# Kernel tuning notes

Hardware: AMD Instinct MI355X
Metric: run time of the kernel (lower is better)

Reference implementation:

```python
import jax, jax.numpy as jnp
import numpy as np

DIM = 768
HEADS = 12
HIDDEN = 4 * DIM
EPS = 1e-5


def _layer_norm(x, g, b):
    mu = jnp.mean(x, axis=-1, keepdims=True)
    var = jnp.mean(jnp.square(x - mu), axis=-1, keepdims=True)
    return (x - mu) * jax.lax.rsqrt(var + EPS) * g + b


def setup_inputs() -> dict:
    key = jax.random.key(0)
    ks = jax.random.split(key, 10)
    B, N, C = 16, 1024, DIM
    s = lambda fan: 1.0 / np.sqrt(fan)
    return {
        "x": jax.random.normal(ks[0], (B, N, C), dtype=jnp.float32),
        "ln1_g": jnp.ones((C,), jnp.float32),
        "ln1_b": jnp.zeros((C,), jnp.float32),
        "qkv_w": jax.random.normal(ks[1], (C, 3 * C), jnp.float32) * s(C),
        "qkv_b": jnp.zeros((3 * C,), jnp.float32),
        "proj_w": jax.random.normal(ks[2], (C, C), jnp.float32) * s(C),
        "proj_b": jnp.zeros((C,), jnp.float32),
        "ln2_g": jnp.ones((C,), jnp.float32),
        "ln2_b": jnp.zeros((C,), jnp.float32),
        "fc1_w": jax.random.normal(ks[3], (C, HIDDEN), jnp.float32) * s(C),
        "fc1_b": jnp.zeros((HIDDEN,), jnp.float32),
        "fc2_w": jax.random.normal(ks[4], (HIDDEN, C), jnp.float32) * s(HIDDEN),
        "fc2_b": jnp.zeros((C,), jnp.float32),
    }


def reference(x, ln1_g, ln1_b, qkv_w, qkv_b, proj_w, proj_b,
              ln2_g, ln2_b, fc1_w, fc1_b, fc2_w, fc2_b):
    B, N, C = x.shape
    Hd = C // HEADS
    scale = Hd ** -0.5

    # --- attention branch (pre-norm) ---
    h = _layer_norm(x, ln1_g, ln1_b)
    qkv = h @ qkv_w + qkv_b                       # [B,N,3C]
    qkv = qkv.reshape(B, N, 3, HEADS, Hd).transpose(2, 0, 3, 1, 4)
    q, k, v = qkv[0], qkv[1], qkv[2]              # [B,H,N,Hd]
    attn = jnp.einsum("bhqd,bhkd->bhqk", q, k) * scale
    attn = jax.nn.softmax(attn, axis=-1)
    o = jnp.einsum("bhqk,bhkd->bhqd", attn, v)    # [B,H,N,Hd]
    o = o.transpose(0, 2, 1, 3).reshape(B, N, C)
    x = x + (o @ proj_w + proj_b)

    # --- MLP branch (pre-norm) ---
    h = _layer_norm(x, ln2_g, ln2_b)
    h = jax.nn.gelu(h @ fc1_w + fc1_b, approximate=False)
    x = x + (h @ fc2_w + fc2_b)
    return x
```

## Files before the change

### kernel.cpp

```cpp
#include <hip/hip_runtime.h>

typedef __bf16 bf16x8 __attribute__((ext_vector_type(8)));
typedef __bf16 bf16x4 __attribute__((ext_vector_type(4)));
typedef float f32x4 __attribute__((ext_vector_type(4)));
typedef float f32x16 __attribute__((ext_vector_type(16)));

#define MFMA16(a,b,c) __builtin_amdgcn_mfma_f32_16x16x32_bf16((a),(b),(c),0,0,0)
#define MFMA32(a,b,c) __builtin_amdgcn_mfma_f32_32x32x16_bf16((a),(b),(c),0,0,0)
#define EXP2R(x) __builtin_amdgcn_exp2f(x)

#define BB   16
#define SEQ  1024
#define CD   768
#define NHD  12
#define HDD  64
#define HID  3072
#define MT   (BB*SEQ)

__device__ __forceinline__ void gload16(const void* g, void* l) {
    __builtin_amdgcn_global_load_lds(
        (const __attribute__((address_space(1))) void*)g,
        (__attribute__((address_space(3))) void*)l, 16, 0, 0);
}

__device__ __forceinline__ unsigned pk2(float lo, float hi) {
    unsigned short a = __builtin_bit_cast(unsigned short, (__bf16)lo);
    unsigned short b = __builtin_bit_cast(unsigned short, (__bf16)hi);
    return (unsigned)a | ((unsigned)b << 16);
}

__device__ __forceinline__ float fast_gelu(float x) {
    float u = x * x * x;
    float y = fmaf(0.044715f, u, x);
    float e = EXP2R(-2.3022083f * y);
    return x * __builtin_amdgcn_rcpf(1.0f + e);
}

__global__ __launch_bounds__(256)
void transpose_w(const float* __restrict__ W, __bf16* __restrict__ WT, int R, int C)
{
    __shared__ float t[32][33];
    int tc = C >> 5;
    int bid = blockIdx.x;
    int br = bid / tc, bc = bid % tc;
    int x = threadIdx.x & 31, y = threadIdx.x >> 5;
#pragma unroll
    for (int i = 0; i < 4; ++i)
        t[y + 8*i][x] = W[(size_t)(br*32 + y + 8*i)*C + bc*32 + x];
    __syncthreads();
#pragma unroll
    for (int i = 0; i < 4; ++i)
        WT[(size_t)(bc*32 + y + 8*i)*R + br*32 + x] = (__bf16)t[x][y + 8*i];
}

__global__ __launch_bounds__(256)
void ln_kernel(const float* __restrict__ xin, const float* __restrict__ g,
               const float* __restrict__ bb, __bf16* out)
{
    int row = blockIdx.x * 4 + (threadIdx.x >> 6);
    int lane = threadIdx.x & 63;
    const float* xr = xin + (size_t)row * CD + lane * 4;
    float4 v0 = *(const float4*)(xr);
    float4 v1 = *(const float4*)(xr + 256);
    float4 v2 = *(const float4*)(xr + 512);
    float s = v0.x+v0.y+v0.z+v0.w + v1.x+v1.y+v1.z+v1.w + v2.x+v2.y+v2.z+v2.w;
#pragma unroll
    for (int off = 1; off < 64; off <<= 1) s += __shfl_xor(s, off);
    float mu = s * (1.0f/768.0f);
    float q =
        (v0.x-mu)*(v0.x-mu)+(v0.y-mu)*(v0.y-mu)+(v0.z-mu)*(v0.z-mu)+(v0.w-mu)*(v0.w-mu)+
        (v1.x-mu)*(v1.x-mu)+(v1.y-mu)*(v1.y-mu)+(v1.z-mu)*(v1.z-mu)+(v1.w-mu)*(v1.w-mu)+
        (v2.x-mu)*(v2.x-mu)+(v2.y-mu)*(v2.y-mu)+(v2.z-mu)*(v2.z-mu)+(v2.w-mu)*(v2.w-mu);
#pragma unroll
    for (int off = 1; off < 64; off <<= 1) q += __shfl_xor(q, off);
    float rstd = rsqrtf(q * (1.0f/768.0f) + 1e-5f);

    __bf16* orow = out + (size_t)row * CD + lane * 4;
#pragma unroll
    for (int p = 0; p < 3; ++p) {
        float4 xv = (p == 0) ? v0 : (p == 1) ? v1 : v2;
        float4 gv = *(const float4*)(g  + p*256 + lane*4);
        float4 bv = *(const float4*)(bb + p*256 + lane*4);
        bf16x4 ov;
        ov[0] = (__bf16)((xv.x-mu)*rstd*gv.x + bv.x);
        ov[1] = (__bf16)((xv.y-mu)*rstd*gv.y + bv.y);
        ov[2] = (__bf16)((xv.z-mu)*rstd*gv.z + bv.z);
        ov[3] = (__bf16)((xv.w-mu)*rstd*gv.w + bv.w);
        *(bf16x4*)(orow + p*256) = ov;
    }
}

template<int EPI>
__global__ __launch_bounds__(512)
void gemm_bt(const __bf16* __restrict__ A, const __bf16* __restrict__ BT,
             const float* __restrict__ bias,
             const float* res, float* outf,
             __bf16* __restrict__ outb,
             __bf16* __restrict__ qb, __bf16* __restrict__ kb, __bf16* __restrict__ vb,
             int M, int N, int K)
{
    __shared__ alignas(16) __bf16 lsA[2][128*64];
    __shared__ alignas(16) __bf16 lsB[2][128*64];

    int nbn = N >> 7;
    int nwg = (M >> 7) * nbn;
    int bid = (int)blockIdx.x;
    int cpx = nwg >> 3;
    int sw = (bid & 7) * cpx + (bid >> 3);
    int bm = sw / nbn, bn = sw % nbn;
    int row0 = bm << 7, col0 = bn << 7;

    int tid = threadIdx.x;
    int lane = tid & 63, w = tid >> 6;
    int wr = w >> 2, wc = w & 3;
    int lr = lane & 15, lg = lane >> 4;

    f32x4 acc[4][2] = {};
    int swz = (lr & 7) << 4;

    auto stage = [&](int buf, int ktE) {
#pragma unroll
        for (int i = 0; i < 2; ++i) {
            int s = tid*16 + (i << 13);
            int r = s >> 7;
            int ch = ((s >> 4) & 7) ^ (r & 7);
            gload16(A  + (size_t)(row0 + r)*K + (ktE + ch*8),
                    (char*)lsA + buf*16384 + w*1024 + (i << 13));
            gload16(BT + (size_t)(col0 + r)*K + (ktE + ch*8),
                    (char*)lsB + buf*16384 + w*1024 + (i << 13));
        }
    };

    int nkt = K >> 6;
    stage(0, 0);
    __syncthreads();
    int cur = 0;

    for (int kt = 0; kt < nkt; ++kt) {
        if (kt + 1 < nkt) stage(cur ^ 1, (kt + 1) << 6);

        const char* lA = (const char*)lsA + cur*16384;
        const char* lB = (const char*)lsB + cur*16384;
#pragma unroll
        for (int ks = 0; ks < 2; ++ks) {
            int cb = (ks*64 + lg*16) ^ swz;
            bf16x8 af[4], bfv[2];
#pragma unroll
            for (int m = 0; m < 4; ++m)
                af[m] = *(const bf16x8*)(lA + (wr*64 + m*16 + lr)*128 + cb);
#pragma unroll
            for (int n = 0; n < 2; ++n)
                bfv[n] = *(const bf16x8*)(lB + (wc*32 + n*16 + lr)*128 + cb);
#pragma unroll
            for (int m = 0; m < 4; ++m)
#pragma unroll
                for (int n = 0; n < 2; ++n)
                    acc[m][n] = MFMA16(af[m], bfv[n], acc[m][n]);
        }
        __syncthreads();
        cur ^= 1;
    }

    int rbase = row0 + wr*64 + lg*4;
    int cbase = col0 + wc*32 + lr;
#pragma unroll
    for (int n = 0; n < 2; ++n) {
        int col = cbase + n*16;
        float bv = bias[col];
        if constexpr (EPI == 0) {
            int which = col / CD;
            int c2 = col - which * CD;
            int head = c2 >> 6, d = c2 & 63;
#pragma unroll
            for (int m = 0; m < 4; ++m) {
                int r0 = rbase + m*16;
                int b = r0 >> 10, nn = r0 & 1023;
                if (which == 2) {
                    bf16x4 pv;
#pragma unroll
                    for (int j = 0; j < 4; ++j) pv[j] = (__bf16)(acc[m][n][j] + bv);
                    *(bf16x4*)&vb[(((size_t)b*NHD + head)*HDD + d)*SEQ + nn] = pv;
                } else {
                    __bf16* dst = (which == 0) ? qb : kb;
#pragma unroll
                    for (int j = 0; j < 4; ++j)
                        dst[(((size_t)b*NHD + head)*SEQ + nn + j)*HDD + d] =
                            (__bf16)(acc[m][n][j] + bv);
                }
            }
        } else {
#pragma unroll
            for (int m = 0; m < 4; ++m) {
                int rr = rbase + m*16;
#pragma unroll
                for (int j = 0; j < 4; ++j) {
                    float val = acc[m][n][j] + bv;
                    int r = rr + j;
                    if constexpr (EPI == 1) {
                        outf[(size_t)r*N + col] = res[(size_t)r*N + col] + val;
                    } else {
                        outb[(size_t)r*N + col] = (__bf16)fast_gelu(val);
                    }
                }
            }
        }
    }
}

__global__ __launch_bounds__(256)
void attn_kernel(const __bf16* __restrict__ q, const __bf16* __restrict__ k,
                 const __bf16* __restrict__ vT, __bf16* __restrict__ o)
{
    __shared__ alignas(16) __bf16 kls[2][64*64];
    __shared__ alignas(16) __bf16 vls[2][64*64];

    int bid = blockIdx.x;
    int u = bid >> 3, x = bid & 7;
    int bh = x*24 + (u >> 3);
    int qt = u & 7;
    int b = bh / NHD, hh = bh % NHD;
    int tid = threadIdx.x, lane = tid & 63, w = tid >> 6;
    int lq = lane & 31, h = lane >> 5;

    int qg = qt*128 + w*32 + lq;
    const __bf16* qp = q + ((size_t)bh*SEQ + qg)*HDD + h*8;
    bf16x8 qf[4];
#pragma unroll
    for (int s = 0; s < 4; ++s) qf[s] = *(const bf16x8*)(qp + s*16);

    const __bf16* kbase = k  + (size_t)bh*SEQ*HDD;
    const __bf16* vbase = vT + (size_t)bh*HDD*SEQ;

    int srow0 = tid >> 3;
    int scol0 = ((tid & 7) ^ (srow0 & 7)) * 8;
    int srow1 = srow0 + 32;

    auto stage = [&](int buf, int kv) {
        char* kl = (char*)kls + buf*8192 + w*1024;
        char* vl = (char*)vls + buf*8192 + w*1024;
        gload16(kbase + (size_t)(kv + srow0)*HDD + scol0, kl);
        gload16(kbase + (size_t)(kv + srow1)*HDD + scol0, kl + 4096);
        gload16(vbase + (size_t)srow0*SEQ + kv + scol0, vl);
        gload16(vbase + (size_t)srow1*SEQ + kv + scol0, vl + 4096);
    };

    const float SCL2 = 0.125f * 1.44269504f;
    const float NB   = -12.0f * SCL2;
    float lrun = 0.f;
    f32x16 oa0 = {}, oa1 = {};

    stage(0, 0);
    __syncthreads();
    int cur = 0;
    int rswz = (lq & 7) << 4;

    for (int kt = 0; kt < SEQ/64; ++kt) {
        if (kt + 1 < SEQ/64) stage(cur ^ 1, (kt + 1)*64);

        const char* kc = (const char*)kls + cur*8192;
        const char* vc = (const char*)vls + cur*8192;

        bf16x8 ka0[4], ka1[4];
#pragma unroll
        for (int s = 0; s < 4; ++s) {
            int bc = (h*16 + s*32) ^ rswz;
            ka0[s] = *(const bf16x8*)(kc + lq*128 + bc);
            ka1[s] = *(const bf16x8*)(kc + (lq + 32)*128 + bc);
        }
        bf16x8 vf0[4], vf1[4];
#pragma unroll
        for (int g = 0; g < 4; ++g) {
            int bc = (h*16 + g*32) ^ rswz;
            vf0[g] = *(const bf16x8*)(vc + lq*128 + bc);
            vf1[g] = *(const bf16x8*)(vc + (lq + 32)*128 + bc);
        }

        f32x16 s0 = {}, s1 = {};
        __builtin_amdgcn_s_setprio(1);
#pragma unroll
        for (int s = 0; s < 4; ++s) {
            s0 = MFMA32(ka0[s], qf[s], s0);
            s1 = MFMA32(ka1[s], qf[s], s1);
        }
        __builtin_amdgcn_s_setprio(0);

#pragma unroll
        for (int i = 0; i < 16; ++i) s0[i] = EXP2R(fmaf(s0[i], SCL2, NB));
#pragma unroll
        for (int i = 0; i < 16; ++i) s1[i] = EXP2R(fmaf(s1[i], SCL2, NB));
        float a8[8];
#pragma unroll
        for (int i = 0; i < 8; ++i)
            a8[i] = (s0[i] + s0[i + 8]) + (s1[i] + s1[i + 8]);
        float s4a = (a8[0] + a8[1]) + (a8[2] + a8[3]);
        float s4b = (a8[4] + a8[5]) + (a8[6] + a8[7]);
        lrun += s4a + s4b;

#pragma unroll
        for (int t = 0; t < 2; ++t) {
            const f32x16& sp = t ? s1 : s0;
            unsigned d0 = pk2(sp[ 0], sp[ 1]);
            unsigned d1 = pk2(sp[ 2], sp[ 3]);
            unsigned d2 = pk2(sp[ 4], sp[ 5]);
            unsigned d3 = pk2(sp[ 6], sp[ 7]);
            unsigned d4 = pk2(sp[ 8], sp[ 9]);
            unsigned d5 = pk2(sp[10], sp[11]);
            unsigned d6 = pk2(sp[12], sp[13]);
            unsigned d7 = pk2(sp[14], sp[15]);
            unsigned pd0 = __shfl_xor(d0, 32), pd1 = __shfl_xor(d1, 32);
            unsigned pd2 = __shfl_xor(d2, 32), pd3 = __shfl_xor(d3, 32);
            unsigned pd4 = __shfl_xor(d4, 32), pd5 = __shfl_xor(d5, 32);
            unsigned pd6 = __shfl_xor(d6, 32), pd7 = __shfl_xor(d7, 32);
            union { unsigned u[4]; bf16x8 v; } f0, f1;
            f0.u[0] = h ? pd2 : d0;
            f0.u[1] = h ? pd3 : d1;
            f0.u[2] = h ? d2 : pd0;
            f0.u[3] = h ? d3 : pd1;
            f1.u[0] = h ? pd6 : d4;
            f1.u[1] = h ? pd7 : d5;
            f1.u[2] = h ? d6 : pd4;
            f1.u[3] = h ? d7 : pd5;
            __builtin_amdgcn_s_setprio(1);
            oa0 = MFMA32(vf0[t*2 + 0], f0.v, oa0);
            oa1 = MFMA32(vf1[t*2 + 0], f0.v, oa1);
            oa0 = MFMA32(vf0[t*2 + 1], f1.v, oa0);
            oa1 = MFMA32(vf1[t*2 + 1], f1.v, oa1);
            __builtin_amdgcn_s_setprio(0);
        }

        __syncthreads();
        cur ^= 1;
    }

    lrun += __shfl_xor(lrun, 32);
    float inv = __builtin_amdgcn_rcpf(lrun);
    oa0 = oa0 * inv;
    oa1 = oa1 * inv;
    __bf16* orow = o + ((size_t)b*SEQ + qg)*CD + hh*HDD;
#pragma unroll
    for (int dt = 0; dt < 2; ++dt) {
        f32x16 oa = dt ? oa1 : oa0;
        unsigned d0 = pk2(oa[ 0], oa[ 1]);
        unsigned d1 = pk2(oa[ 2], oa[ 3]);
        unsigned d2 = pk2(oa[ 4], oa[ 5]);
        unsigned d3 = pk2(oa[ 6], oa[ 7]);
        unsigned d4 = pk2(oa[ 8], oa[ 9]);
        unsigned d5 = pk2(oa[10], oa[11]);
        unsigned d6 = pk2(oa[12], oa[13]);
        unsigned d7 = pk2(oa[14], oa[15]);
        unsigned pd0 = __shfl_xor(d0, 32), pd1 = __shfl_xor(d1, 32);
        unsigned pd2 = __shfl_xor(d2, 32), pd3 = __shfl_xor(d3, 32);
        unsigned pd4 = __shfl_xor(d4, 32), pd5 = __shfl_xor(d5, 32);
        unsigned pd6 = __shfl_xor(d6, 32), pd7 = __shfl_xor(d7, 32);
        union { unsigned u[4]; bf16x8 v; } g0, g1;
        g0.u[0] = h ? pd2 : d0;
        g0.u[1] = h ? pd3 : d1;
        g0.u[2] = h ? d2 : pd0;
        g0.u[3] = h ? d3 : pd1;
        g1.u[0] = h ? pd6 : d4;
        g1.u[1] = h ? pd7 : d5;
        g1.u[2] = h ? d6 : pd4;
        g1.u[3] = h ? d7 : pd5;
        *(bf16x8*)(orow + dt*32 +  0 + h*8) = g0.v;
        *(bf16x8*)(orow + dt*32 + 16 + h*8) = g1.v;
    }
}

extern "C" void kernel_launch(void* const* d_in, const int* in_sizes, int n_in,
                              void* d_out, int out_size, void* d_ws, size_t ws_size,
                              hipStream_t stream)
{
    const float* x     = (const float*)d_in[0];
    const float* ln1g  = (const float*)d_in[1];
    const float* ln1b  = (const float*)d_in[2];
    const float* qkvw  = (const float*)d_in[3];
    const float* qkvb  = (const float*)d_in[4];
    const float* projw = (const float*)d_in[5];
    const float* projb = (const float*)d_in[6];
    const float* ln2g  = (const float*)d_in[7];
    const float* ln2b  = (const float*)d_in[8];
    const float* fc1w  = (const float*)d_in[9];
    const float* fc1b  = (const float*)d_in[10];
    const float* fc2w  = (const float*)d_in[11];
    const float* fc2b  = (const float*)d_in[12];
    float* out = (float*)d_out;

    char* p = (char*)d_ws;
    auto alloc = [&](size_t bytes) { char* r = p; p += (bytes + 255) & ~(size_t)255; return r; };
    __bf16* wqkvT  = (__bf16*)alloc((size_t)3*CD*CD*2);
    __bf16* wprojT = (__bf16*)alloc((size_t)CD*CD*2);
    __bf16* wfc1T  = (__bf16*)alloc((size_t)HID*CD*2);
    __bf16* wfc2T  = (__bf16*)alloc((size_t)CD*HID*2);
    __bf16* hbuf   = (__bf16*)alloc((size_t)MT*CD*2);
    __bf16* qbuf   = (__bf16*)alloc((size_t)BB*NHD*SEQ*HDD*2);
    __bf16* kbuf   = (__bf16*)alloc((size_t)BB*NHD*SEQ*HDD*2);
    __bf16* vtbuf  = (__bf16*)alloc((size_t)BB*NHD*SEQ*HDD*2);
    (void)alloc((size_t)BB*NHD*SEQ*HDD*2);
    __bf16* hhbuf  = qbuf;

    transpose_w<<<(CD/32)*(3*CD/32), 256, 0, stream>>>(qkvw,  wqkvT, CD, 3*CD);
    transpose_w<<<(CD/32)*(CD/32),   256, 0, stream>>>(projw, wprojT, CD, CD);
    transpose_w<<<(CD/32)*(HID/32),  256, 0, stream>>>(fc1w,  wfc1T, CD, HID);
    transpose_w<<<(HID/32)*(CD/32),  256, 0, stream>>>(fc2w,  wfc2T, HID, CD);

    ln_kernel<<<MT/4, 256, 0, stream>>>(x, ln1g, ln1b, hbuf);

    gemm_bt<0><<<(MT/128)*(3*CD/128), 512, 0, stream>>>(
        hbuf, wqkvT, qkvb, nullptr, nullptr, nullptr, qbuf, kbuf, vtbuf, MT, 3*CD, CD);

    attn_kernel<<<BB*NHD*8, 256, 0, stream>>>(qbuf, kbuf, vtbuf, hbuf);

    gemm_bt<1><<<(MT/128)*(CD/128), 512, 0, stream>>>(
        hbuf, wprojT, projb, x, out, nullptr, nullptr, nullptr, nullptr, MT, CD, CD);

    ln_kernel<<<MT/4, 256, 0, stream>>>(out, ln2g, ln2b, hbuf);

    gemm_bt<2><<<(MT/128)*(HID/128), 512, 0, stream>>>(
        hbuf, wfc1T, fc1b, nullptr, nullptr, hhbuf, nullptr, nullptr, nullptr, MT, HID, CD);

    gemm_bt<1><<<(MT/128)*(CD/128), 512, 0, stream>>>(
        hhbuf, wfc2T, fc2b, out, out, nullptr, nullptr, nullptr, nullptr, MT, CD, HID);
}
```

Baseline: 463.7 us.

## Add 256x256-tile GEMM for MLP layers and fuse weight transposes with LN1

Adds a new GEMM kernel with 256x256 output tiles per 512-thread workgroup. It double-buffers LDS with staged prefetch interleaved into the MFMA loop, and uses it for the fc1 and fc2 GEMMs to raise data reuse per tile. Separately, the four weight-transpose launches and the first layer norm are merged into one prep kernel to cut launch overhead. The larger tiles use 128 KB of LDS and more accumulator registers, and the fc2 GEMM gets only 192 workgroups, which may underfill the GPU.

```diff
diff --git a/kernel.cpp b/kernel.cpp
--- a/kernel.cpp
+++ b/kernel.cpp
@@ -8,6 +8,7 @@
 #define MFMA16(a,b,c) __builtin_amdgcn_mfma_f32_16x16x32_bf16((a),(b),(c),0,0,0)
 #define MFMA32(a,b,c) __builtin_amdgcn_mfma_f32_32x32x16_bf16((a),(b),(c),0,0,0)
 #define EXP2R(x) __builtin_amdgcn_exp2f(x)
+#define SBAR() asm volatile("s_barrier" ::: "memory")
 
 #define BB   16
 #define SEQ  1024
@@ -36,12 +37,11 @@
     return x * __builtin_amdgcn_rcpf(1.0f + e);
 }
 
-__global__ __launch_bounds__(256)
-void transpose_w(const float* __restrict__ W, __bf16* __restrict__ WT, int R, int C)
-{
-    __shared__ float t[32][33];
+__device__ __forceinline__ void transpose_body(
+    const float* __restrict__ W, __bf16* __restrict__ WT, int R, int C, int bid,
+    float (*t)[33])
+{
     int tc = C >> 5;
-    int bid = blockIdx.x;
     int br = bid / tc, bc = bid % tc;
     int x = threadIdx.x & 31, y = threadIdx.x >> 5;
 #pragma unroll
@@ -53,11 +53,11 @@
         WT[(size_t)(bc*32 + y + 8*i)*R + br*32 + x] = (__bf16)t[x][y + 8*i];
 }
 
-__global__ __launch_bounds__(256)
-void ln_kernel(const float* __restrict__ xin, const float* __restrict__ g,
-               const float* __restrict__ bb, __bf16* out)
-{
-    int row = blockIdx.x * 4 + (threadIdx.x >> 6);
+__device__ __forceinline__ void ln_body(
+    const float* __restrict__ xin, const float* __restrict__ g,
+    const float* __restrict__ bb, __bf16* out, int bid)
+{
+    int row = bid * 4 + ((int)threadIdx.x >> 6);
     int lane = threadIdx.x & 63;
     const float* xr = xin + (size_t)row * CD + lane * 4;
     float4 v0 = *(const float4*)(xr);
@@ -90,6 +90,31 @@
     }
 }
 
+__global__ __launch_bounds__(256)
+void prep_kernel(const float* qkvw, const float* projw, const float* fc1w, const float* fc2w,
+                 __bf16* wqkvT, __bf16* wprojT, __bf16* wfc1T, __bf16* wfc2T,
+                 const float* x, const float* g1, const float* b1, __bf16* hbuf)
+{
+    __shared__ float t[32][33];
+    int bid = blockIdx.x;
+    if (bid < 1728) { transpose_body(qkvw,  wqkvT,  CD,  3*CD, bid, t); return; }
+    bid -= 1728;
+    if (bid < 576)  { transpose_body(projw, wprojT, CD,  CD,   bid, t); return; }
+    bid -= 576;
+    if (bid < 2304) { transpose_body(fc1w,  wfc1T,  CD,  HID,  bid, t); return; }
+    bid -= 2304;
+    if (bid < 2304) { transpose_body(fc2w,  wfc2T,  HID, CD,   bid, t); return; }
+    bid -= 2304;
+    ln_body(x, g1, b1, hbuf, bid);
+}
+
+__global__ __launch_bounds__(256)
+void ln_kernel(const float* __restrict__ xin, const float* __restrict__ g,
+               const float* __restrict__ bb, __bf16* out)
+{
+    ln_body(xin, g, bb, out, blockIdx.x);
+}
+
 template<int EPI>
 __global__ __launch_bounds__(512)
 void gemm_bt(const __bf16* __restrict__ A, const __bf16* __restrict__ BT,
@@ -201,6 +226,118 @@
                     } else {
                         outb[(size_t)r*N + col] = (__bf16)fast_gelu(val);
                     }
+                }
+            }
+        }
+    }
+}
+
+template<int EPI>
+__global__ __launch_bounds__(512, 2)
+void gemm256(const __bf16* __restrict__ A, const __bf16* __restrict__ BT,
+             const float* __restrict__ bias,
+             const float* res, float* outf, __bf16* __restrict__ outb,
+             int M, int N, int K)
+{
+    __shared__ alignas(16) __bf16 lsA[2][256*64];
+    __shared__ alignas(16) __bf16 lsB[2][256*64];
+
+    int nbn = N >> 8;
+    int nwg = (M >> 8) * nbn;
+    int bid = (int)blockIdx.x;
+    int cpx = nwg >> 3;
+    int sw = (bid & 7) * cpx + (bid >> 3);
+    int bm = sw / nbn, bn = sw % nbn;
+    int row0 = bm << 8, col0 = bn << 8;
+
+    int tid = threadIdx.x;
+    int lane = tid & 63, w = tid >> 6;
+    int wr = w >> 2, wc = w & 3;
+    int lr = lane & 15, lg = lane >> 4;
+    int swz = (lr & 7) << 4;
+
+    const __bf16* Ab = A  + (size_t)row0 * K;
+    const __bf16* Bb = BT + (size_t)col0 * K;
+
+    auto stageH = [&](__bf16* ls, const __bf16* src, int half, int ktE) {
+#pragma unroll
+        for (int rd = 0; rd < 2; ++rd) {
+            int s = tid*16 + (rd << 13);
+            int r = s >> 7;
+            int ch = ((s >> 4) & 7) ^ (r & 7);
+            gload16(src + (size_t)(half*128 + r)*K + (ktE + ch*8),
+                    (char*)ls + half*16384 + (rd << 13) + w*1024);
+        }
+    };
+
+    f32x4 acc[8][4] = {};
+
+    int nkt = K >> 6;
+    stageH(lsA[0], Ab, 0, 0); stageH(lsA[0], Ab, 1, 0);
+    stageH(lsB[0], Bb, 0, 0); stageH(lsB[0], Bb, 1, 0);
+
+    for (int t = 0; t < nkt; ++t) {
+        int slot = t & 1, nslot = slot ^ 1;
+        int kn = (t + 1) << 6;
+        bool pf = (t + 1 < nkt);
+
+        if (pf) {
+            stageH(lsA[nslot], Ab, 0, kn);
+            asm volatile("s_waitcnt vmcnt(2)" ::: "memory");
+        } else {
+            asm volatile("s_waitcnt vmcnt(0)" ::: "memory");
+        }
+        SBAR();
+
+        const char* lA = (const char*)lsA[slot];
+        const char* lB = (const char*)lsB[slot];
+
+#pragma unroll
+        for (int ks = 0; ks < 2; ++ks) {
+            int cb = (ks*64 + lg*16) ^ swz;
+            bf16x8 bfr[4];
+#pragma unroll
+            for (int n = 0; n < 4; ++n)
+                bfr[n] = *(const bf16x8*)(lB + (wc*64 + n*16 + lr)*128 + cb);
+#pragma unroll
+            for (int mh = 0; mh < 2; ++mh) {
+                bf16x8 afr[4];
+#pragma unroll
+                for (int mm = 0; mm < 4; ++mm)
+                    afr[mm] = *(const bf16x8*)(lA + (wr*128 + mh*64 + mm*16 + lr)*128 + cb);
+                if (pf) {
+                    if (ks == 0 && mh == 0) stageH(lsA[nslot], Ab, 1, kn);
+                    else if (ks == 0 && mh == 1) stageH(lsB[nslot], Bb, 0, kn);
+                    else if (ks == 1 && mh == 0) stageH(lsB[nslot], Bb, 1, kn);
+                }
+                __builtin_amdgcn_s_setprio(1);
+#pragma unroll
+                for (int mm = 0; mm < 4; ++mm)
+#pragma unroll
+                    for (int n = 0; n < 4; ++n)
+                        acc[mh*4 + mm][n] = MFMA16(afr[mm], bfr[n], acc[mh*4 + mm][n]);
+                __builtin_amdgcn_s_setprio(0);
+            }
+        }
+        SBAR();
+    }
+
+    int rb = row0 + wr*128 + lg*4;
+    int cb2 = col0 + wc*64 + lr;
+#pragma unroll
+    for (int n = 0; n < 4; ++n) {
+        int col = cb2 + n*16;
+        float bv = bias[col];
+#pragma unroll
+        for (int m = 0; m < 8; ++m) {
+#pragma unroll
+            for (int j = 0; j < 4; ++j) {
+                int r = rb + m*16 + j;
+                float val = acc[m][n][j] + bv;
+                if constexpr (EPI == 1) {
+                    outf[(size_t)r*N + col] = res[(size_t)r*N + col] + val;
+                } else {
+                    outb[(size_t)r*N + col] = (__bf16)fast_gelu(val);
                 }
             }
         }
@@ -398,12 +535,8 @@
     (void)alloc((size_t)BB*NHD*SEQ*HDD*2);
     __bf16* hhbuf  = qbuf;
 
-    transpose_w<<<(CD/32)*(3*CD/32), 256, 0, stream>>>(qkvw,  wqkvT, CD, 3*CD);
-    transpose_w<<<(CD/32)*(CD/32),   256, 0, stream>>>(projw, wprojT, CD, CD);
-    transpose_w<<<(CD/32)*(HID/32),  256, 0, stream>>>(fc1w,  wfc1T, CD, HID);
-    transpose_w<<<(HID/32)*(CD/32),  256, 0, stream>>>(fc2w,  wfc2T, HID, CD);
-
-    ln_kernel<<<MT/4, 256, 0, stream>>>(x, ln1g, ln1b, hbuf);
+    prep_kernel<<<1728 + 576 + 2304 + 2304 + MT/4, 256, 0, stream>>>(
+        qkvw, projw, fc1w, fc2w, wqkvT, wprojT, wfc1T, wfc2T, x, ln1g, ln1b, hbuf);
 
     gemm_bt<0><<<(MT/128)*(3*CD/128), 512, 0, stream>>>(
         hbuf, wqkvT, qkvb, nullptr, nullptr, nullptr, qbuf, kbuf, vtbuf, MT, 3*CD, CD);
@@ -415,9 +548,9 @@
 
     ln_kernel<<<MT/4, 256, 0, stream>>>(out, ln2g, ln2b, hbuf);
 
-    gemm_bt<2><<<(MT/128)*(HID/128), 512, 0, stream>>>(
-        hbuf, wfc1T, fc1b, nullptr, nullptr, hhbuf, nullptr, nullptr, nullptr, MT, HID, CD);
-
-    gemm_bt<1><<<(MT/128)*(CD/128), 512, 0, stream>>>(
-        hhbuf, wfc2T, fc2b, out, out, nullptr, nullptr, nullptr, nullptr, MT, CD, HID);
-}
+    gemm256<2><<<(MT/256)*(HID/256), 512, 0, stream>>>(
+        hbuf, wfc1T, fc1b, nullptr, nullptr, hhbuf, MT, HID, CD);
+
+    gemm256<1><<<(MT/256)*(CD/256), 512, 0, stream>>>(
+        hhbuf, wfc2T, fc2b, out, out, nullptr, MT, CD, HID);
+}
```

Measured after the change: 462.4 us. About the same (-0.3%).

## Triple-buffer GEMM LDS staging and fuse weight transposes with first layernorm

Applied to the files above, without the earlier changes.

The GEMM moves from double to triple-buffered LDS staging. It prefetches two K-tiles ahead and uses explicit vmcnt waits with raw s_barrier instead of __syncthreads, so more global-load latency is hidden. Separately, the four weight-transpose launches and the first layernorm are merged into one prep kernel to cut launch overhead. The larger LDS footprint of 96KB per block may reduce the number of resident blocks per CU.

```diff
diff --git a/kernel.cpp b/kernel.cpp
--- a/kernel.cpp
+++ b/kernel.cpp
@@ -8,6 +8,7 @@
 #define MFMA16(a,b,c) __builtin_amdgcn_mfma_f32_16x16x32_bf16((a),(b),(c),0,0,0)
 #define MFMA32(a,b,c) __builtin_amdgcn_mfma_f32_32x32x16_bf16((a),(b),(c),0,0,0)
 #define EXP2R(x) __builtin_amdgcn_exp2f(x)
+#define SBAR() asm volatile("s_barrier" ::: "memory")
 
 #define BB   16
 #define SEQ  1024
@@ -36,12 +37,11 @@
     return x * __builtin_amdgcn_rcpf(1.0f + e);
 }
 
-__global__ __launch_bounds__(256)
-void transpose_w(const float* __restrict__ W, __bf16* __restrict__ WT, int R, int C)
-{
-    __shared__ float t[32][33];
+__device__ __forceinline__ void transpose_body(
+    const float* __restrict__ W, __bf16* __restrict__ WT, int R, int C, int bid,
+    float (*t)[33])
+{
     int tc = C >> 5;
-    int bid = blockIdx.x;
     int br = bid / tc, bc = bid % tc;
     int x = threadIdx.x & 31, y = threadIdx.x >> 5;
 #pragma unroll
@@ -53,11 +53,11 @@
         WT[(size_t)(bc*32 + y + 8*i)*R + br*32 + x] = (__bf16)t[x][y + 8*i];
 }
 
-__global__ __launch_bounds__(256)
-void ln_kernel(const float* __restrict__ xin, const float* __restrict__ g,
-               const float* __restrict__ bb, __bf16* out)
-{
-    int row = blockIdx.x * 4 + (threadIdx.x >> 6);
+__device__ __forceinline__ void ln_body(
+    const float* __restrict__ xin, const float* __restrict__ g,
+    const float* __restrict__ bb, __bf16* out, int bid)
+{
+    int row = bid * 4 + ((int)threadIdx.x >> 6);
     int lane = threadIdx.x & 63;
     const float* xr = xin + (size_t)row * CD + lane * 4;
     float4 v0 = *(const float4*)(xr);
@@ -90,6 +90,31 @@
     }
 }
 
+__global__ __launch_bounds__(256)
+void prep_kernel(const float* qkvw, const float* projw, const float* fc1w, const float* fc2w,
+                 __bf16* wqkvT, __bf16* wprojT, __bf16* wfc1T, __bf16* wfc2T,
+                 const float* x, const float* g1, const float* b1, __bf16* hbuf)
+{
+    __shared__ float t[32][33];
+    int bid = blockIdx.x;
+    if (bid < 1728) { transpose_body(qkvw,  wqkvT,  CD,  3*CD, bid, t); return; }
+    bid -= 1728;
+    if (bid < 576)  { transpose_body(projw, wprojT, CD,  CD,   bid, t); return; }
+    bid -= 576;
+    if (bid < 2304) { transpose_body(fc1w,  wfc1T,  CD,  HID,  bid, t); return; }
+    bid -= 2304;
+    if (bid < 2304) { transpose_body(fc2w,  wfc2T,  HID, CD,   bid, t); return; }
+    bid -= 2304;
+    ln_body(x, g1, b1, hbuf, bid);
+}
+
+__global__ __launch_bounds__(256)
+void ln_kernel(const float* __restrict__ xin, const float* __restrict__ g,
+               const float* __restrict__ bb, __bf16* out)
+{
+    ln_body(xin, g, bb, out, blockIdx.x);
+}
+
 template<int EPI>
 __global__ __launch_bounds__(512)
 void gemm_bt(const __bf16* __restrict__ A, const __bf16* __restrict__ BT,
@@ -99,8 +124,8 @@
              __bf16* __restrict__ qb, __bf16* __restrict__ kb, __bf16* __restrict__ vb,
              int M, int N, int K)
 {
-    __shared__ alignas(16) __bf16 lsA[2][128*64];
-    __shared__ alignas(16) __bf16 lsB[2][128*64];
+    __shared__ alignas(16) __bf16 lsA[3][128*64];
+    __shared__ alignas(16) __bf16 lsB[3][128*64];
 
     int nbn = N >> 7;
     int nwg = (M >> 7) * nbn;
@@ -133,11 +158,19 @@
 
     int nkt = K >> 6;
     stage(0, 0);
-    __syncthreads();
-    int cur = 0;
+    stage(1, 64);
 
     for (int kt = 0; kt < nkt; ++kt) {
-        if (kt + 1 < nkt) stage(cur ^ 1, (kt + 1) << 6);
+        int cur = kt % 3;
+        if (kt + 2 < nkt) {
+            stage((kt + 2) % 3, (kt + 2) << 6);
+            asm volatile("s_waitcnt vmcnt(8)" ::: "memory");
+        } else if (kt + 1 < nkt) {
+            asm volatile("s_waitcnt vmcnt(4)" ::: "memory");
+        } else {
+            asm volatile("s_waitcnt vmcnt(0)" ::: "memory");
+        }
+        SBAR();
 
         const char* lA = (const char*)lsA + cur*16384;
         const char* lB = (const char*)lsB + cur*16384;
@@ -157,8 +190,7 @@
                 for (int n = 0; n < 2; ++n)
                     acc[m][n] = MFMA16(af[m], bfv[n], acc[m][n]);
         }
-        __syncthreads();
-        cur ^= 1;
+        SBAR();
     }
 
     int rbase = row0 + wr*64 + lg*4;
@@ -398,12 +430,8 @@
     (void)alloc((size_t)BB*NHD*SEQ*HDD*2);
     __bf16* hhbuf  = qbuf;
 
-    transpose_w<<<(CD/32)*(3*CD/32), 256, 0, stream>>>(qkvw,  wqkvT, CD, 3*CD);
-    transpose_w<<<(CD/32)*(CD/32),   256, 0, stream>>>(projw, wprojT, CD, CD);
-    transpose_w<<<(CD/32)*(HID/32),  256, 0, stream>>>(fc1w,  wfc1T, CD, HID);
-    transpose_w<<<(HID/32)*(CD/32),  256, 0, stream>>>(fc2w,  wfc2T, HID, CD);
-
-    ln_kernel<<<MT/4, 256, 0, stream>>>(x, ln1g, ln1b, hbuf);
+    prep_kernel<<<1728 + 576 + 2304 + 2304 + MT/4, 256, 0, stream>>>(
+        qkvw, projw, fc1w, fc2w, wqkvT, wprojT, wfc1T, wfc2T, x, ln1g, ln1b, hbuf);
 
     gemm_bt<0><<<(MT/128)*(3*CD/128), 512, 0, stream>>>(
         hbuf, wqkvT, qkvb, nullptr, nullptr, nullptr, qbuf, kbuf, vtbuf, MT, 3*CD, CD);
```

New measurement: 603.2 us. +30.1%, slower.
